# Optimization experiments

Hardware: AMD Instinct MI355X
Metric: run time of the kernel (lower is better)

The kernel has to match this reference:

```python
import jax, jax.numpy as jnp
import numpy as np

DIM = 1024
INNER = DIM // 2
DSTATE = 8
KSZ = 3
DTRANK = max(INNER // 8, 4)
B, L = 4, 4096


def setup_inputs() -> dict:
    key = jax.random.key(0)
    ks = jax.random.split(key, 8)
    s = 0.02
    x = jax.random.normal(ks[0], (B, L, DIM), dtype=jnp.float32)
    W_in = jax.random.normal(ks[1], (DIM, DIM), dtype=jnp.float32) * s
    Kx = jax.random.normal(ks[2], (INNER, 1, KSZ), dtype=jnp.float32) * 0.1
    Kz = jax.random.normal(ks[3], (INNER, 1, KSZ), dtype=jnp.float32) * 0.1
    W_xproj = jax.random.normal(ks[4], (DTRANK + 2 * DSTATE, INNER), dtype=jnp.float32) * s
    W_dt = jax.random.normal(ks[5], (INNER, DTRANK), dtype=jnp.float32) * s
    # dt bias: inverse_softplus of exp(linspace(log dt_min, log dt_max))
    dt_init = jnp.exp(jnp.linspace(jnp.log(0.02), jnp.log(0.2), INNER))
    b_dt = jnp.log(jnp.expm1(dt_init)).astype(jnp.float32)
    A_log = jnp.log(jnp.tile(jnp.arange(1, DSTATE + 1, dtype=jnp.float32), (INNER, 1)))
    D = jnp.ones((INNER,), dtype=jnp.float32)
    W_out = jax.random.normal(ks[6], (DIM, DIM), dtype=jnp.float32) * s
    return {"x": x, "W_in": W_in, "Kx": Kx, "Kz": Kz, "W_xproj": W_xproj,
            "W_dt": W_dt, "b_dt": b_dt, "A_log": A_log, "D": D, "W_out": W_out}


def _dwconv_silu(u, kern):
    # u: [B,L,C], kern: [C,1,K] depthwise (groups=C), 'same' padding
    c = u.shape[-1]
    v = jnp.transpose(u, (0, 2, 1))  # [B,C,L]
    v = jax.lax.conv_general_dilated(v, kern, (1,), [(KSZ // 2, KSZ // 2)],
                                     dimension_numbers=("NCH", "OIH", "NCH"),
                                     feature_group_count=c)
    return jax.nn.silu(jnp.transpose(v, (0, 2, 1)))


def _forward(x, W_in, Kx, Kz, W_xproj, W_dt, b_dt, A_log, D, W_out):
    h = jnp.einsum("bld,ed->ble", x, W_in)  # Linear(dim,dim), no bias
    xb, zb = jnp.split(h, 2, axis=-1)       # [B,L,INNER] each
    xb = _dwconv_silu(xb, Kx)
    zb = _dwconv_silu(zb, Kz)
    proj = jnp.einsum("blc,oc->blo", xb, W_xproj)
    dt_raw = proj[..., :DTRANK]
    b_raw = proj[..., DTRANK:DTRANK + DSTATE]
    c_raw = proj[..., DTRANK + DSTATE:]
    delta = jnp.clip(jax.nn.softplus(jnp.einsum("blr,cr->blc", dt_raw, W_dt) + b_dt), 1e-4, 1.0)  # [B,L,C]
    b_term = jnp.tanh(b_raw)  # [B,L,N]
    c_term = jnp.tanh(c_raw)  # [B,L,N]
    a = jax.nn.softplus(A_log) + 1e-4  # [C,N]
    decay = jnp.clip(jnp.exp(-delta[..., None] * a), 1e-4, 1.0)        # [B,L,C,N]
    drive = (1.0 - decay) * (b_term[:, :, None, :] * xb[..., None])    # [B,L,C,N]

    def step(state, inp):
        dec_t, drv_t, c_t, x_t = inp  # [B,C,N], [B,C,N], [B,N], [B,C]
        state = dec_t * state + drv_t
        y = jnp.sum(state * c_t[:, None, :], axis=-1) + D * x_t  # [B,C]
        return state, y

    tm = lambda t: jnp.moveaxis(t, 1, 0)  # time-major
    state0 = jnp.zeros((x.shape[0], INNER, DSTATE), dtype=jnp.float32)
    _, ys = jax.lax.scan(step, state0, (tm(decay), tm(drive), tm(c_term), tm(xb)))
    y = jnp.moveaxis(ys, 0, 1)  # [B,L,INNER]
    return jnp.einsum("bld,ed->ble", jnp.concatenate([y, zb], axis=-1), W_out)


def reference(x, W_in, Kx, Kz, W_xproj, W_dt, b_dt, A_log, D, W_out):
    return _forward(x, W_in, Kx, Kz, W_xproj, W_dt, b_dt, A_log, D, W_out)
```

## Files before the change

kernel.cpp:

```cpp
#include <hip/hip_runtime.h>


using bf16x8 = __attribute__((ext_vector_type(8))) short;
using f32x4  = __attribute__((ext_vector_type(4))) float;

__device__ __forceinline__ unsigned short f2bf(float f) {
  unsigned int u = __float_as_uint(f);
  u = u + 0x7fffu + ((u >> 16) & 1u);
  return (unsigned short)(u >> 16);
}

__device__ __forceinline__ float fsoftplus(float x) {
  return (x > 15.f) ? x : __logf(1.f + __expf(x));
}

__device__ __forceinline__ float ftanh(float x) {
  float v = fminf(fmaxf(x, -15.f), 15.f);
  float e = __expf(2.f * v);
  return (e - 1.f) / (e + 1.f);
}

__global__ __launch_bounds__(256) void cvt_bf16_kernel(
    const float* __restrict__ in, unsigned short* __restrict__ out, int n4) {
  int i = blockIdx.x * 256 + threadIdx.x;
  if (i < n4) {
    float4 v = ((const float4*)in)[i];
    ushort4 o;
    o.x = f2bf(v.x); o.y = f2bf(v.y); o.z = f2bf(v.z); o.w = f2bf(v.w);
    ((ushort4*)out)[i] = o;
  }
}

__global__ __launch_bounds__(256) void cvt_wxp_kernel(
    const float* __restrict__ Wx, unsigned short* __restrict__ out) {
  int i = blockIdx.x * 256 + threadIdx.x;
  int row = i >> 9;
  out[i] = (row < 80) ? f2bf(Wx[i]) : (unsigned short)0;
}

__global__ __launch_bounds__(256) void gemm_bt_bf16(
    const unsigned short* __restrict__ A,
    const unsigned short* __restrict__ B,
    float* __restrict__ C, int M, int N, int K) {
  __shared__ short As[128 * 32];
  __shared__ short Bs[128 * 32];
  const int m0 = blockIdx.x * 128;
  const int n0 = blockIdx.y * 128;
  const int lane = threadIdx.x & 63;
  const int wv = threadIdx.x >> 6;
  const int wm = (wv >> 1) * 64;
  const int wn = (wv & 1) * 64;
  f32x4 acc[4][4] = {};
  const int row_a = wv * 32 + (lane >> 2);
  const int koff = (lane & 3) * 8;
  const unsigned short* gA = A + (size_t)(m0 + row_a) * K + koff;
  const unsigned short* gB = B + (size_t)(n0 + row_a) * K + koff;
  short* lA = &As[(wv * 32) * 32];
  short* lB = &Bs[(wv * 32) * 32];
  const int r = lane & 15;
  const int q = lane >> 4;
  for (int k0 = 0; k0 < K; k0 += 32) {
    __syncthreads();
    __builtin_amdgcn_global_load_lds((const __attribute__((address_space(1))) void*)(const void*)gA,
                                     (__attribute__((address_space(3))) void*)(void*)lA, 16, 0, 0);
    __builtin_amdgcn_global_load_lds((const __attribute__((address_space(1))) void*)(const void*)(gA + 16 * K),
                                     (__attribute__((address_space(3))) void*)(void*)(lA + 16 * 32), 16, 0, 0);
    __builtin_amdgcn_global_load_lds((const __attribute__((address_space(1))) void*)(const void*)gB,
                                     (__attribute__((address_space(3))) void*)(void*)lB, 16, 0, 0);
    __builtin_amdgcn_global_load_lds((const __attribute__((address_space(1))) void*)(const void*)(gB + 16 * K),
                                     (__attribute__((address_space(3))) void*)(void*)(lB + 16 * 32), 16, 0, 0);
    gA += 32; gB += 32;
    __syncthreads();
    bf16x8 av[4], bv[4];
#pragma unroll
    for (int i = 0; i < 4; ++i)
      av[i] = *(const bf16x8*)&As[(wm + i * 16 + r) * 32 + q * 8];
#pragma unroll
    for (int j = 0; j < 4; ++j)
      bv[j] = *(const bf16x8*)&Bs[(wn + j * 16 + r) * 32 + q * 8];
#pragma unroll
    for (int i = 0; i < 4; ++i)
#pragma unroll
      for (int j = 0; j < 4; ++j)
        acc[i][j] = __builtin_amdgcn_mfma_f32_16x16x32_bf16(av[i], bv[j], acc[i][j], 0, 0, 0);
  }
#pragma unroll
  for (int i = 0; i < 4; ++i)
#pragma unroll
    for (int j = 0; j < 4; ++j)
#pragma unroll
      for (int t = 0; t < 4; ++t)
        C[(size_t)(m0 + wm + i * 16 + q * 4 + t) * N + (n0 + wn + j * 16 + r)] = acc[i][j][t];
}

__device__ __forceinline__ void g256_stage(short* lds, int slot,
    const unsigned short* sp, int ktIdx, int wvLds, int K) {
  const unsigned short* s = sp + ktIdx * 64;
  __builtin_amdgcn_global_load_lds((const __attribute__((address_space(1))) void*)s,
      (__attribute__((address_space(3))) void*)(lds + slot * 8192 + wvLds), 16, 0, 0);
  __builtin_amdgcn_global_load_lds((const __attribute__((address_space(1))) void*)(s + (size_t)64 * K),
      (__attribute__((address_space(3))) void*)(lds + slot * 8192 + 4096 + wvLds), 16, 0, 0);
}

template <int PAR, int MH, int NHLO, bool RA, bool RB, int SSLOT, bool VM, bool HINT>
__device__ __forceinline__ void g256_phase(
    short* lds, int aSlotOff, int bSlotOff, int aoff, int boff, int wvLds,
    bf16x8 (&av)[4][2], bf16x8 (&bv)[4][2], f32x4 (&acc)[8][4],
    const unsigned short* sp, int ktIdx, int K) {
  if (RA) {
#pragma unroll
    for (int ii = 0; ii < 4; ++ii) {
      av[ii][0] = *(const bf16x8*)&lds[PAR * 4 * 8192 + aSlotOff + MH * 4096 + ii * 1024 + aoff];
      av[ii][1] = *(const bf16x8*)&lds[PAR * 4 * 8192 + aSlotOff + MH * 4096 + ii * 1024 + (aoff ^ 32)];
    }
  }
  if (RB) {
#pragma unroll
    for (int jj = 0; jj < 2; ++jj) {
      bv[NHLO + jj][0] = *(const bf16x8*)&lds[(PAR * 4 + 2) * 8192 + bSlotOff + (NHLO + jj) * 1024 + boff];
      bv[NHLO + jj][1] = *(const bf16x8*)&lds[(PAR * 4 + 2) * 8192 + bSlotOff + (NHLO + jj) * 1024 + (boff ^ 32)];
    }
  }
  g256_stage(lds, SSLOT, sp, ktIdx, wvLds, K);
  if (HINT) asm volatile("s_waitcnt lgkmcnt(8)");
  if (VM) asm volatile("s_waitcnt vmcnt(4)" ::: "memory");
  __builtin_amdgcn_s_barrier();
  asm volatile("s_waitcnt lgkmcnt(0)" ::: "memory");
  __builtin_amdgcn_s_setprio(1);
#pragma unroll
  for (int ii = 0; ii < 4; ++ii)
#pragma unroll
    for (int jj = 0; jj < 2; ++jj) {
      acc[MH * 4 + ii][NHLO + jj] = __builtin_amdgcn_mfma_f32_16x16x32_bf16(
          av[ii][0], bv[NHLO + jj][0], acc[MH * 4 + ii][NHLO + jj], 0, 0, 0);
      acc[MH * 4 + ii][NHLO + jj] = __builtin_amdgcn_mfma_f32_16x16x32_bf16(
          av[ii][1], bv[NHLO + jj][1], acc[MH * 4 + ii][NHLO + jj], 0, 0, 0);
    }
  __builtin_amdgcn_s_setprio(0);
  __builtin_amdgcn_s_barrier();
}

__global__ __launch_bounds__(512, 2) void gemm256_bt(
    const unsigned short* __restrict__ A,
    const unsigned short* __restrict__ B,
    float* __restrict__ C, int M, int N, int K) {
  __shared__ short lds[8 * 8192];
  const int nmt = M >> 8;
  const int bid = blockIdx.x;
  const int g = nmt >> 3;
  const int xcd = bid & 7;
  const int loc = bid >> 3;
  const int mtile = xcd * g + (loc % g);
  const int ntile = loc / g;
  const int m0 = mtile << 8, n0 = ntile << 8;
  const int tid = threadIdx.x;
  const int w = tid >> 6, lane = tid & 63;
  const int r = lane & 15, q = lane >> 4;
  const int wrow = w >> 2, wcol = w & 3;
  const int srow = tid >> 3;
  const int scol = ((tid & 7) ^ (srow & 7)) << 3;
  const unsigned short* pA0 = A + (size_t)(m0 + srow) * K + scol;
  const unsigned short* pA1 = A + (size_t)(m0 + 128 + srow) * K + scol;
  const unsigned short* pB0 = B + (size_t)(n0 + srow) * K + scol;
  const unsigned short* pB1 = B + (size_t)(n0 + 128 + srow) * K + scol;
  const int wvLds = w * 512;
  const int aSlotOff = wrow * 8192;
  const int bSlotOff = (wcol >> 1) * 8192;
  const int swzc = (q * 8) ^ ((r & 7) << 3);
  const int aoff = r * 64 + swzc;
  const int boff = (wcol & 1) * 4096 + r * 64 + swzc;
  bf16x8 av[4][2], bv[4][2];
  f32x4 acc[8][4] = {};
  const int NT = K >> 6;
  const int NI = NT >> 1;
  g256_stage(lds, 0, pA0, 0, wvLds, K);
  g256_stage(lds, 1, pA1, 0, wvLds, K);
  g256_stage(lds, 2, pB0, 0, wvLds, K);
  g256_stage(lds, 3, pB1, 0, wvLds, K);
  g256_stage(lds, 6, pB0, 1, wvLds, K);
  g256_stage(lds, 7, pB1, 1, wvLds, K);
  asm volatile("s_waitcnt vmcnt(4)" ::: "memory");
  __builtin_amdgcn_s_barrier();
#pragma unroll 1
  for (int it = 0; it < NI; ++it) {
    const int ktO  = 2 * it + 1;
    const int ktE2 = (2 * it + 2 < NT) ? 2 * it + 2 : NT - 1;
    const int ktO2 = (2 * it + 3 < NT) ? 2 * it + 3 : NT - 1;
    g256_phase<0, 0, 0, true,  true,  4, false, true >(lds, aSlotOff, bSlotOff, aoff, boff, wvLds, av, bv, acc, pA0, ktO,  K);
    g256_phase<0, 0, 2, false, true,  5, false, false>(lds, aSlotOff, bSlotOff, aoff, boff, wvLds, av, bv, acc, pA1, ktO,  K);
    g256_phase<0, 1, 2, true,  false, 2, false, false>(lds, aSlotOff, bSlotOff, aoff, boff, wvLds, av, bv, acc, pB0, ktE2, K);
    g256_phase<0, 1, 0, false, false, 0, true,  false>(lds, aSlotOff, bSlotOff, aoff, boff, wvLds, av, bv, acc, pA0, ktE2, K);
    g256_phase<1, 0, 0, true,  true,  1, false, true >(lds, aSlotOff, bSlotOff, aoff, boff, wvLds, av, bv, acc, pA1, ktE2, K);
    g256_phase<1, 0, 2, false, true,  3, false, false>(lds, aSlotOff, bSlotOff, aoff, boff, wvLds, av, bv, acc, pB1, ktE2, K);
    g256_phase<1, 1, 2, true,  false, 6, false, false>(lds, aSlotOff, bSlotOff, aoff, boff, wvLds, av, bv, acc, pB0, ktO2, K);
    g256_phase<1, 1, 0, false, false, 7, true,  false>(lds, aSlotOff, bSlotOff, aoff, boff, wvLds, av, bv, acc, pB1, ktO2, K);
  }
  asm volatile("s_waitcnt vmcnt(0) lgkmcnt(0)" ::: "memory");
  float* Cw = C + (size_t)(m0 + wrow * 128) * N + n0 + wcol * 64;
#pragma unroll
  for (int ii = 0; ii < 8; ++ii)
#pragma unroll
    for (int jj = 0; jj < 4; ++jj)
#pragma unroll
      for (int t = 0; t < 4; ++t)
        Cw[(size_t)(ii * 16 + q * 4 + t) * N + jj * 16 + r] = acc[ii][jj][t];
}

__global__ __launch_bounds__(256) void conv_silu_kernel(
    const float* __restrict__ h, const float* __restrict__ Kx, const float* __restrict__ Kz,
    float* __restrict__ xb, unsigned short* __restrict__ xbbf,
    unsigned short* __restrict__ cat) {
  int tid = blockIdx.x * 256 + threadIdx.x;
  int ch = tid & 1023;
  int bl = tid >> 10;
  int l = bl & 4095;
  float k0, k1, k2;
  int c;
  if (ch < 512) { c = ch;       k0 = Kx[c * 3]; k1 = Kx[c * 3 + 1]; k2 = Kx[c * 3 + 2]; }
  else          { c = ch - 512; k0 = Kz[c * 3]; k1 = Kz[c * 3 + 1]; k2 = Kz[c * 3 + 2]; }
  size_t idx = (size_t)bl * 1024 + ch;
  float um = (l > 0)    ? h[idx - 1024] : 0.f;
  float u0 = h[idx];
  float up = (l < 4095) ? h[idx + 1024] : 0.f;
  float v = um * k0 + u0 * k1 + up * k2;
  float o = v / (1.f + __expf(-v));
  if (ch < 512) { xb[(size_t)bl * 512 + c] = o; xbbf[(size_t)bl * 512 + c] = f2bf(o); }
  else          cat[idx] = f2bf(o);
}

__global__ __launch_bounds__(256) void prep_dtbc_kernel(
    const float* __restrict__ proj, unsigned short* __restrict__ dtr,
    float* __restrict__ bterm, float* __restrict__ cterm) {
  int i = blockIdx.x * 256 + threadIdx.x;
  int row = i >> 7, col = i & 127;
  float v = proj[i];
  if (col < 64)      dtr[row * 64 + col] = f2bf(v);
  else if (col < 72) bterm[row * 8 + (col - 64)] = ftanh(v);
  else if (col < 80) cterm[row * 8 + (col - 72)] = ftanh(v);
}

__global__ __launch_bounds__(256) void scan_p1(
    const float* __restrict__ draw, const float* __restrict__ bterm,
    const float* __restrict__ xb, const float* __restrict__ A_log,
    const float* __restrict__ bdt,
    float* __restrict__ Aprod, float* __restrict__ Bpart) {
  int tid = threadIdx.x;
  int gid = blockIdx.x;
  int chunk = gid & 127, half = (gid >> 7) & 1, b = gid >> 8;
  int c = half * 256 + tid;
  float4 a0 = *(const float4*)&A_log[c * 8];
  float4 a1 = *(const float4*)&A_log[c * 8 + 4];
  float na[8] = {a0.x, a0.y, a0.z, a0.w, a1.x, a1.y, a1.z, a1.w};
#pragma unroll
  for (int s = 0; s < 8; ++s) na[s] = -(fsoftplus(na[s]) + 1e-4f);
  float bb = bdt[c];
  int l0 = chunk * 32;
  size_t base  = ((size_t)b * 4096 + l0) * 512 + c;
  size_t bbase = ((size_t)b * 4096 + l0) * 8;
  float S[8] = {}, Ap[8] = {1.f, 1.f, 1.f, 1.f, 1.f, 1.f, 1.f, 1.f};
  for (int i = 0; i < 32; ++i) {
    float dr = draw[base] + bb;
    float xv = xb[base];
    float delta = fminf(fmaxf(fsoftplus(dr), 1e-4f), 1.f);
    float4 bt0 = *(const float4*)&bterm[bbase];
    float4 bt1 = *(const float4*)&bterm[bbase + 4];
    float bt[8] = {bt0.x, bt0.y, bt0.z, bt0.w, bt1.x, bt1.y, bt1.z, bt1.w};
#pragma unroll
    for (int s = 0; s < 8; ++s) {
      float dec = fminf(fmaxf(__expf(delta * na[s]), 1e-4f), 1.f);
      float btx = bt[s] * xv;
      S[s] = dec * S[s] + (btx - dec * btx);
      Ap[s] *= dec;
    }
    base += 512; bbase += 8;
  }
  size_t o = (size_t)chunk * 16384 + ((size_t)(b * 512 + c)) * 8;
  *(float4*)&Aprod[o]     = make_float4(Ap[0], Ap[1], Ap[2], Ap[3]);
  *(float4*)&Aprod[o + 4] = make_float4(Ap[4], Ap[5], Ap[6], Ap[7]);
  *(float4*)&Bpart[o]     = make_float4(S[0], S[1], S[2], S[3]);
  *(float4*)&Bpart[o + 4] = make_float4(S[4], S[5], S[6], S[7]);
}

__global__ __launch_bounds__(256) void scan_p2(
    const float* __restrict__ Aprod, const float* __restrict__ Bpart,
    float* __restrict__ initst) {
  int t = blockIdx.x * 256 + threadIdx.x;
  float st = 0.f;
  for (int ch = 0; ch < 128; ++ch) {
    size_t o = (size_t)ch * 16384 + t;
    initst[o] = st;
    st = Aprod[o] * st + Bpart[o];
  }
}

__global__ __launch_bounds__(256) void scan_p3(
    const float* __restrict__ draw, const float* __restrict__ bterm,
    const float* __restrict__ cterm, const float* __restrict__ xb,
    const float* __restrict__ A_log, const float* __restrict__ bdt,
    const float* __restrict__ Dp,
    const float* __restrict__ initst, unsigned short* __restrict__ cat) {
  int tid = threadIdx.x;
  int gid = blockIdx.x;
  int chunk = gid & 127, half = (gid >> 7) & 1, b = gid >> 8;
  int c = half * 256 + tid;
  float4 a0 = *(const float4*)&A_log[c * 8];
  float4 a1 = *(const float4*)&A_log[c * 8 + 4];
  float na[8] = {a0.x, a0.y, a0.z, a0.w, a1.x, a1.y, a1.z, a1.w};
#pragma unroll
  for (int s = 0; s < 8; ++s) na[s] = -(fsoftplus(na[s]) + 1e-4f);
  float bb = bdt[c];
  float Dv = Dp[c];
  size_t o = (size_t)chunk * 16384 + ((size_t)(b * 512 + c)) * 8;
  float4 s0 = *(const float4*)&initst[o];
  float4 s1 = *(const float4*)&initst[o + 4];
  float S[8] = {s0.x, s0.y, s0.z, s0.w, s1.x, s1.y, s1.z, s1.w};
  int l0 = chunk * 32;
  size_t base  = ((size_t)b * 4096 + l0) * 512 + c;
  size_t bbase = ((size_t)b * 4096 + l0) * 8;
  size_t cbase = ((size_t)b * 4096 + l0) * 1024 + c;
  for (int i = 0; i < 32; ++i) {
    float dr = draw[base] + bb;
    float xv = xb[base];
    float delta = fminf(fmaxf(fsoftplus(dr), 1e-4f), 1.f);
    float4 bt0 = *(const float4*)&bterm[bbase];
    float4 bt1 = *(const float4*)&bterm[bbase + 4];
    float4 ct0 = *(const float4*)&cterm[bbase];
    float4 ct1 = *(const float4*)&cterm[bbase + 4];
    float bt[8] = {bt0.x, bt0.y, bt0.z, bt0.w, bt1.x, bt1.y, bt1.z, bt1.w};
    float ct[8] = {ct0.x, ct0.y, ct0.z, ct0.w, ct1.x, ct1.y, ct1.z, ct1.w};
    float acc = Dv * xv;
#pragma unroll
    for (int s = 0; s < 8; ++s) {
      float dec = fminf(fmaxf(__expf(delta * na[s]), 1e-4f), 1.f);
      float btx = bt[s] * xv;
      S[s] = dec * S[s] + (btx - dec * btx);
      acc += S[s] * ct[s];
    }
    cat[cbase] = f2bf(acc);
    base += 512; bbase += 8; cbase += 1024;
  }
}

extern "C" void kernel_launch(void* const* d_in, const int* in_sizes, int n_in,
                              void* d_out, int out_size, void* d_ws, size_t ws_size,
                              hipStream_t stream) {
  (void)in_sizes; (void)n_in; (void)out_size; (void)ws_size;
  const float* x       = (const float*)d_in[0];
  const float* W_in    = (const float*)d_in[1];
  const float* Kx      = (const float*)d_in[2];
  const float* Kz      = (const float*)d_in[3];
  const float* W_xproj = (const float*)d_in[4];
  const float* W_dt    = (const float*)d_in[5];
  const float* b_dt    = (const float*)d_in[6];
  const float* A_log   = (const float*)d_in[7];
  const float* Dp      = (const float*)d_in[8];
  const float* W_out   = (const float*)d_in[9];
  float* out = (float*)d_out;

  char* w = (char*)d_ws;
  unsigned short* xbf  = (unsigned short*)(w);
  float* xb    = (float*)(w + 33554432);
  float* draw  = (float*)(w + 67108864);
  float* bterm = (float*)(w + 100663296);
  float* cterm = (float*)(w + 101187584);
  float* Aprod = (float*)(w + 101711872);
  float* Bpart = (float*)(w + 110100480);
  float* initst = (float*)(w + 118489088);
  unsigned short* winbf  = (unsigned short*)(w + 126877696);
  unsigned short* woutbf = (unsigned short*)(w + 128974848);
  unsigned short* dtr    = (unsigned short*)(w + 131072000);
  unsigned short* wxp_bf = (unsigned short*)(w + 133169152);
  unsigned short* wd_bf  = (unsigned short*)(w + 133300224);
  unsigned short* xbbf = (unsigned short*)Aprod;
  float* proj = draw;
  float* h = out;

  cvt_bf16_kernel<<<16384, 256, 0, stream>>>(x, xbf, 4194304);
  cvt_bf16_kernel<<<1024, 256, 0, stream>>>(W_in, winbf, 262144);
  cvt_bf16_kernel<<<1024, 256, 0, stream>>>(W_out, woutbf, 262144);
  cvt_bf16_kernel<<<32, 256, 0, stream>>>(W_dt, wd_bf, 8192);
  cvt_wxp_kernel<<<256, 256, 0, stream>>>(W_xproj, wxp_bf);

  gemm256_bt<<<256, 512, 0, stream>>>(xbf, winbf, h, 16384, 1024, 1024);

  conv_silu_kernel<<<65536, 256, 0, stream>>>(h, Kx, Kz, xb, xbbf, xbf );

  gemm_bt_bf16<<<dim3(128, 1), 256, 0, stream>>>(xbbf, wxp_bf, proj, 16384, 128, 512);
  prep_dtbc_kernel<<<8192, 256, 0, stream>>>(proj, dtr, bterm, cterm);
  gemm_bt_bf16<<<dim3(128, 4), 256, 0, stream>>>(dtr, wd_bf, draw, 16384, 512, 64);

  scan_p1<<<1024, 256, 0, stream>>>(draw, bterm, xb, A_log, b_dt, Aprod, Bpart);
  scan_p2<<<64, 256, 0, stream>>>(Aprod, Bpart, initst);
  scan_p3<<<1024, 256, 0, stream>>>(draw, bterm, cterm, xb, A_log, b_dt, Dp, initst, xbf );

  gemm256_bt<<<256, 512, 0, stream>>>(xbf, woutbf, out, 16384, 1024, 1024);
}
```

Before: 347.5 us.

## Fuse epilogues into small GEMMs, vectorize conv, and re-pipeline big GEMM LDS reads

The prep_dtbc pass is folded into the x-projection GEMM epilogue, which now writes the bf16 dt rows and the tanh of the B/C terms directly. The softplus and clip for delta move into the dt GEMM epilogue, so the two scan kernels read delta instead of recomputing it. The depthwise conv+SiLU kernel now handles four channels per thread with float4 loads, and scan_p2 batches its loads eight chunks at a time. The 256-tile GEMM is re-pipelined so LDS fragment reads for the next phase are issued after the current MFMAs and one more stage is prefetched. Together these aim to cut kernel launches, intermediate traffic and repeated transcendental math, but the GEMM reordering raises register pressure and depends on correct waitcnt bookkeeping.

```diff
diff --git a/kernel.cpp b/kernel.cpp
--- a/kernel.cpp
+++ b/kernel.cpp
@@ -38,9 +38,73 @@
   out[i] = (row < 80) ? f2bf(Wx[i]) : (unsigned short)0;
 }
 
-__global__ __launch_bounds__(256) void gemm_bt_bf16(
+
+__global__ __launch_bounds__(256) void gemm_proj128(
     const unsigned short* __restrict__ A,
     const unsigned short* __restrict__ B,
+    unsigned short* __restrict__ dtr, float* __restrict__ bterm,
+    float* __restrict__ cterm, int M, int N, int K) {
+  __shared__ short As[128 * 32];
+  __shared__ short Bs[128 * 32];
+  const int m0 = blockIdx.x * 128;
+  const int lane = threadIdx.x & 63;
+  const int wv = threadIdx.x >> 6;
+  const int wm = (wv >> 1) * 64;
+  const int wn = (wv & 1) * 64;
+  f32x4 acc[4][4] = {};
+  const int row_a = wv * 32 + (lane >> 2);
+  const int koff = (lane & 3) * 8;
+  const unsigned short* gA = A + (size_t)(m0 + row_a) * K + koff;
+  const unsigned short* gB = B + (size_t)row_a * K + koff;
+  short* lA = &As[(wv * 32) * 32];
+  short* lB = &Bs[(wv * 32) * 32];
+  const int r = lane & 15;
+  const int q = lane >> 4;
+  for (int k0 = 0; k0 < K; k0 += 32) {
+    __syncthreads();
+    __builtin_amdgcn_global_load_lds((const __attribute__((address_space(1))) void*)(const void*)gA,
+                                     (__attribute__((address_space(3))) void*)(void*)lA, 16, 0, 0);
+    __builtin_amdgcn_global_load_lds((const __attribute__((address_space(1))) void*)(const void*)(gA + 16 * K),
+                                     (__attribute__((address_space(3))) void*)(void*)(lA + 16 * 32), 16, 0, 0);
+    __builtin_amdgcn_global_load_lds((const __attribute__((address_space(1))) void*)(const void*)gB,
+                                     (__attribute__((address_space(3))) void*)(void*)lB, 16, 0, 0);
+    __builtin_amdgcn_global_load_lds((const __attribute__((address_space(1))) void*)(const void*)(gB + 16 * K),
+                                     (__attribute__((address_space(3))) void*)(void*)(lB + 16 * 32), 16, 0, 0);
+    gA += 32; gB += 32;
+    __syncthreads();
+    bf16x8 av[4], bv[4];
+#pragma unroll
+    for (int i = 0; i < 4; ++i)
+      av[i] = *(const bf16x8*)&As[(wm + i * 16 + r) * 32 + q * 8];
+#pragma unroll
+    for (int j = 0; j < 4; ++j)
+      bv[j] = *(const bf16x8*)&Bs[(wn + j * 16 + r) * 32 + q * 8];
+#pragma unroll
+    for (int i = 0; i < 4; ++i)
+#pragma unroll
+      for (int j = 0; j < 4; ++j)
+        acc[i][j] = __builtin_amdgcn_mfma_f32_16x16x32_bf16(av[i], bv[j], acc[i][j], 0, 0, 0);
+  }
+#pragma unroll
+  for (int i = 0; i < 4; ++i)
+#pragma unroll
+    for (int j = 0; j < 4; ++j) {
+      const int col = wn + j * 16 + r;
+#pragma unroll
+      for (int t = 0; t < 4; ++t) {
+        const int row = m0 + wm + i * 16 + q * 4 + t;
+        float v = acc[i][j][t];
+        if (col < 64)      dtr[(size_t)row * 64 + col] = f2bf(v);
+        else if (col < 72) bterm[(size_t)row * 8 + (col - 64)] = ftanh(v);
+        else if (col < 80) cterm[(size_t)row * 8 + (col - 72)] = ftanh(v);
+      }
+    }
+}
+
+__global__ __launch_bounds__(256) void gemm_dt128(
+    const unsigned short* __restrict__ A,
+    const unsigned short* __restrict__ B,
+    const float* __restrict__ bdt,
     float* __restrict__ C, int M, int N, int K) {
   __shared__ short As[128 * 32];
   __shared__ short Bs[128 * 32];
@@ -85,12 +149,18 @@
         acc[i][j] = __builtin_amdgcn_mfma_f32_16x16x32_bf16(av[i], bv[j], acc[i][j], 0, 0, 0);
   }
 #pragma unroll
-  for (int i = 0; i < 4; ++i)
-#pragma unroll
-    for (int j = 0; j < 4; ++j)
-#pragma unroll
-      for (int t = 0; t < 4; ++t)
-        C[(size_t)(m0 + wm + i * 16 + q * 4 + t) * N + (n0 + wn + j * 16 + r)] = acc[i][j][t];
+  for (int j = 0; j < 4; ++j) {
+    const int col = n0 + wn + j * 16 + r;
+    const float bb = bdt[col];
+#pragma unroll
+    for (int i = 0; i < 4; ++i)
+#pragma unroll
+      for (int t = 0; t < 4; ++t) {
+        float v = acc[i][j][t] + bb;
+        float delta = fminf(fmaxf(fsoftplus(v), 1e-4f), 1.f);
+        C[(size_t)(m0 + wm + i * 16 + q * 4 + t) * N + col] = delta;
+      }
+  }
 }
 
 __device__ __forceinline__ void g256_stage(short* lds, int slot,
@@ -102,41 +172,51 @@
       (__attribute__((address_space(3))) void*)(lds + slot * 8192 + 4096 + wvLds), 16, 0, 0);
 }
 
-template <int PAR, int MH, int NHLO, bool RA, bool RB, int SSLOT, bool VM, bool HINT>
+template <int MP, int MH, int NL, int SSLOT, bool VM, int RK, int RP>
 __device__ __forceinline__ void g256_phase(
     short* lds, int aSlotOff, int bSlotOff, int aoff, int boff, int wvLds,
     bf16x8 (&av)[4][2], bf16x8 (&bv)[4][2], f32x4 (&acc)[8][4],
     const unsigned short* sp, int ktIdx, int K) {
-  if (RA) {
+  g256_stage(lds, SSLOT, sp, ktIdx, wvLds, K);
+  if (VM) asm volatile("s_waitcnt vmcnt(6)" ::: "memory");
+  __builtin_amdgcn_s_barrier();
+  __builtin_amdgcn_s_setprio(1);
+#pragma unroll
+  for (int ii = 0; ii < 4; ++ii)
+#pragma unroll
+    for (int jj = 0; jj < 2; ++jj) {
+      acc[MH * 4 + ii][NL + jj] = __builtin_amdgcn_mfma_f32_16x16x32_bf16(
+          av[ii][0], bv[NL + jj][0], acc[MH * 4 + ii][NL + jj], 0, 0, 0);
+      acc[MH * 4 + ii][NL + jj] = __builtin_amdgcn_mfma_f32_16x16x32_bf16(
+          av[ii][1], bv[NL + jj][1], acc[MH * 4 + ii][NL + jj], 0, 0, 0);
+    }
+  __builtin_amdgcn_s_setprio(0);
+  if (RK == 2) {
 #pragma unroll
     for (int ii = 0; ii < 4; ++ii) {
-      av[ii][0] = *(const bf16x8*)&lds[PAR * 4 * 8192 + aSlotOff + MH * 4096 + ii * 1024 + aoff];
-      av[ii][1] = *(const bf16x8*)&lds[PAR * 4 * 8192 + aSlotOff + MH * 4096 + ii * 1024 + (aoff ^ 32)];
-    }
-  }
-  if (RB) {
+      av[ii][0] = *(const bf16x8*)&lds[RP * 4 * 8192 + aSlotOff + 4096 + ii * 1024 + aoff];
+      av[ii][1] = *(const bf16x8*)&lds[RP * 4 * 8192 + aSlotOff + 4096 + ii * 1024 + (aoff ^ 32)];
+    }
+  }
+  if (RK >= 3) {
+#pragma unroll
+    for (int ii = 0; ii < 4; ++ii) {
+      av[ii][0] = *(const bf16x8*)&lds[RP * 4 * 8192 + aSlotOff + ii * 1024 + aoff];
+      av[ii][1] = *(const bf16x8*)&lds[RP * 4 * 8192 + aSlotOff + ii * 1024 + (aoff ^ 32)];
+    }
 #pragma unroll
     for (int jj = 0; jj < 2; ++jj) {
-      bv[NHLO + jj][0] = *(const bf16x8*)&lds[(PAR * 4 + 2) * 8192 + bSlotOff + (NHLO + jj) * 1024 + boff];
-      bv[NHLO + jj][1] = *(const bf16x8*)&lds[(PAR * 4 + 2) * 8192 + bSlotOff + (NHLO + jj) * 1024 + (boff ^ 32)];
-    }
-  }
-  g256_stage(lds, SSLOT, sp, ktIdx, wvLds, K);
-  if (HINT) asm volatile("s_waitcnt lgkmcnt(8)");
-  if (VM) asm volatile("s_waitcnt vmcnt(4)" ::: "memory");
-  __builtin_amdgcn_s_barrier();
-  asm volatile("s_waitcnt lgkmcnt(0)" ::: "memory");
-  __builtin_amdgcn_s_setprio(1);
-#pragma unroll
-  for (int ii = 0; ii < 4; ++ii)
-#pragma unroll
-    for (int jj = 0; jj < 2; ++jj) {
-      acc[MH * 4 + ii][NHLO + jj] = __builtin_amdgcn_mfma_f32_16x16x32_bf16(
-          av[ii][0], bv[NHLO + jj][0], acc[MH * 4 + ii][NHLO + jj], 0, 0, 0);
-      acc[MH * 4 + ii][NHLO + jj] = __builtin_amdgcn_mfma_f32_16x16x32_bf16(
-          av[ii][1], bv[NHLO + jj][1], acc[MH * 4 + ii][NHLO + jj], 0, 0, 0);
-    }
-  __builtin_amdgcn_s_setprio(0);
+      bv[jj][0] = *(const bf16x8*)&lds[(RP * 4 + 2) * 8192 + bSlotOff + jj * 1024 + boff];
+      bv[jj][1] = *(const bf16x8*)&lds[(RP * 4 + 2) * 8192 + bSlotOff + jj * 1024 + (boff ^ 32)];
+    }
+  }
+  if (RK == 1 || RK == 4) {
+#pragma unroll
+    for (int jj = 2; jj < 4; ++jj) {
+      bv[jj][0] = *(const bf16x8*)&lds[(RP * 4 + 2) * 8192 + bSlotOff + jj * 1024 + boff];
+      bv[jj][1] = *(const bf16x8*)&lds[(RP * 4 + 2) * 8192 + bSlotOff + jj * 1024 + (boff ^ 32)];
+    }
+  }
   __builtin_amdgcn_s_barrier();
 }
 
@@ -177,23 +257,34 @@
   g256_stage(lds, 1, pA1, 0, wvLds, K);
   g256_stage(lds, 2, pB0, 0, wvLds, K);
   g256_stage(lds, 3, pB1, 0, wvLds, K);
+  g256_stage(lds, 4, pA0, 1, wvLds, K);
   g256_stage(lds, 6, pB0, 1, wvLds, K);
   g256_stage(lds, 7, pB1, 1, wvLds, K);
-  asm volatile("s_waitcnt vmcnt(4)" ::: "memory");
+  asm volatile("s_waitcnt vmcnt(6)" ::: "memory");
   __builtin_amdgcn_s_barrier();
+#pragma unroll
+  for (int ii = 0; ii < 4; ++ii) {
+    av[ii][0] = *(const bf16x8*)&lds[aSlotOff + ii * 1024 + aoff];
+    av[ii][1] = *(const bf16x8*)&lds[aSlotOff + ii * 1024 + (aoff ^ 32)];
+  }
+#pragma unroll
+  for (int jj = 0; jj < 2; ++jj) {
+    bv[jj][0] = *(const bf16x8*)&lds[2 * 8192 + bSlotOff + jj * 1024 + boff];
+    bv[jj][1] = *(const bf16x8*)&lds[2 * 8192 + bSlotOff + jj * 1024 + (boff ^ 32)];
+  }
 #pragma unroll 1
   for (int it = 0; it < NI; ++it) {
-    const int ktO  = 2 * it + 1;
-    const int ktE2 = (2 * it + 2 < NT) ? 2 * it + 2 : NT - 1;
-    const int ktO2 = (2 * it + 3 < NT) ? 2 * it + 3 : NT - 1;
-    g256_phase<0, 0, 0, true,  true,  4, false, true >(lds, aSlotOff, bSlotOff, aoff, boff, wvLds, av, bv, acc, pA0, ktO,  K);
-    g256_phase<0, 0, 2, false, true,  5, false, false>(lds, aSlotOff, bSlotOff, aoff, boff, wvLds, av, bv, acc, pA1, ktO,  K);
-    g256_phase<0, 1, 2, true,  false, 2, false, false>(lds, aSlotOff, bSlotOff, aoff, boff, wvLds, av, bv, acc, pB0, ktE2, K);
-    g256_phase<0, 1, 0, false, false, 0, true,  false>(lds, aSlotOff, bSlotOff, aoff, boff, wvLds, av, bv, acc, pA0, ktE2, K);
-    g256_phase<1, 0, 0, true,  true,  1, false, true >(lds, aSlotOff, bSlotOff, aoff, boff, wvLds, av, bv, acc, pA1, ktE2, K);
-    g256_phase<1, 0, 2, false, true,  3, false, false>(lds, aSlotOff, bSlotOff, aoff, boff, wvLds, av, bv, acc, pB1, ktE2, K);
-    g256_phase<1, 1, 2, true,  false, 6, false, false>(lds, aSlotOff, bSlotOff, aoff, boff, wvLds, av, bv, acc, pB0, ktO2, K);
-    g256_phase<1, 1, 0, false, false, 7, true,  false>(lds, aSlotOff, bSlotOff, aoff, boff, wvLds, av, bv, acc, pB1, ktO2, K);
+    const int ktO = 2 * it + 1;
+    const int kt2 = (2 * it + 2 < NT) ? 2 * it + 2 : NT - 1;
+    const int kt3 = (2 * it + 3 < NT) ? 2 * it + 3 : NT - 1;
+    g256_phase<0,0,0, 5, false, 1, 0>(lds, aSlotOff, bSlotOff, aoff, boff, wvLds, av, bv, acc, pA1, ktO, K);
+    g256_phase<0,0,2, 2, false, 2, 0>(lds, aSlotOff, bSlotOff, aoff, boff, wvLds, av, bv, acc, pB0, kt2, K);
+    g256_phase<0,1,2, 3, false, 0, 0>(lds, aSlotOff, bSlotOff, aoff, boff, wvLds, av, bv, acc, pB1, kt2, K);
+    g256_phase<0,1,0, 0, true,  4, 1>(lds, aSlotOff, bSlotOff, aoff, boff, wvLds, av, bv, acc, pA0, kt2, K);
+    g256_phase<1,0,0, 1, false, 0, 0>(lds, aSlotOff, bSlotOff, aoff, boff, wvLds, av, bv, acc, pA1, kt2, K);
+    g256_phase<1,0,2, 6, false, 2, 1>(lds, aSlotOff, bSlotOff, aoff, boff, wvLds, av, bv, acc, pB0, kt3, K);
+    g256_phase<1,1,2, 7, false, 0, 0>(lds, aSlotOff, bSlotOff, aoff, boff, wvLds, av, bv, acc, pB1, kt3, K);
+    g256_phase<1,1,0, 4, true,  3, 0>(lds, aSlotOff, bSlotOff, aoff, boff, wvLds, av, bv, acc, pA0, kt3, K);
   }
   asm volatile("s_waitcnt vmcnt(0) lgkmcnt(0)" ::: "memory");
   float* Cw = C + (size_t)(m0 + wrow * 128) * N + n0 + wcol * 64;
@@ -206,43 +297,45 @@
         Cw[(size_t)(ii * 16 + q * 4 + t) * N + jj * 16 + r] = acc[ii][jj][t];
 }
 
-__global__ __launch_bounds__(256) void conv_silu_kernel(
+__global__ __launch_bounds__(256) void conv_silu_v4(
     const float* __restrict__ h, const float* __restrict__ Kx, const float* __restrict__ Kz,
     float* __restrict__ xb, unsigned short* __restrict__ xbbf,
     unsigned short* __restrict__ cat) {
   int tid = blockIdx.x * 256 + threadIdx.x;
-  int ch = tid & 1023;
-  int bl = tid >> 10;
+  int c4 = (tid & 255) << 2;
+  int bl = tid >> 8;
   int l = bl & 4095;
-  float k0, k1, k2;
-  int c;
-  if (ch < 512) { c = ch;       k0 = Kx[c * 3]; k1 = Kx[c * 3 + 1]; k2 = Kx[c * 3 + 2]; }
-  else          { c = ch - 512; k0 = Kz[c * 3]; k1 = Kz[c * 3 + 1]; k2 = Kz[c * 3 + 2]; }
-  size_t idx = (size_t)bl * 1024 + ch;
-  float um = (l > 0)    ? h[idx - 1024] : 0.f;
-  float u0 = h[idx];
-  float up = (l < 4095) ? h[idx + 1024] : 0.f;
-  float v = um * k0 + u0 * k1 + up * k2;
-  float o = v / (1.f + __expf(-v));
-  if (ch < 512) { xb[(size_t)bl * 512 + c] = o; xbbf[(size_t)bl * 512 + c] = f2bf(o); }
-  else          cat[idx] = f2bf(o);
-}
-
-__global__ __launch_bounds__(256) void prep_dtbc_kernel(
-    const float* __restrict__ proj, unsigned short* __restrict__ dtr,
-    float* __restrict__ bterm, float* __restrict__ cterm) {
-  int i = blockIdx.x * 256 + threadIdx.x;
-  int row = i >> 7, col = i & 127;
-  float v = proj[i];
-  if (col < 64)      dtr[row * 64 + col] = f2bf(v);
-  else if (col < 72) bterm[row * 8 + (col - 64)] = ftanh(v);
-  else if (col < 80) cterm[row * 8 + (col - 72)] = ftanh(v);
+  const float* Kp; int c;
+  if (c4 < 512) { Kp = Kx; c = c4; } else { Kp = Kz; c = c4 - 512; }
+  const float4* K4 = (const float4*)(Kp + c * 3);
+  float4 ka = K4[0], kb = K4[1], kc = K4[2];
+  size_t idx = (size_t)bl * 1024 + c4;
+  float4 zero = make_float4(0.f, 0.f, 0.f, 0.f);
+  float4 um = (l > 0)    ? *(const float4*)(h + idx - 1024) : zero;
+  float4 u0 = *(const float4*)(h + idx);
+  float4 up = (l < 4095) ? *(const float4*)(h + idx + 1024) : zero;
+  float v0 = um.x * ka.x + u0.x * ka.y + up.x * ka.z;
+  float v1 = um.y * ka.w + u0.y * kb.x + up.y * kb.y;
+  float v2 = um.z * kb.z + u0.z * kb.w + up.z * kc.x;
+  float v3 = um.w * kc.y + u0.w * kc.z + up.w * kc.w;
+  float o0 = v0 / (1.f + __expf(-v0));
+  float o1 = v1 / (1.f + __expf(-v1));
+  float o2 = v2 / (1.f + __expf(-v2));
+  float o3 = v3 / (1.f + __expf(-v3));
+  ushort4 ob;
+  ob.x = f2bf(o0); ob.y = f2bf(o1); ob.z = f2bf(o2); ob.w = f2bf(o3);
+  if (c4 < 512) {
+    size_t xo = (size_t)bl * 512 + c4;
+    *(float4*)(xb + xo) = make_float4(o0, o1, o2, o3);
+    *(ushort4*)(xbbf + xo) = ob;
+  } else {
+    *(ushort4*)(cat + idx) = ob;
+  }
 }
 
 __global__ __launch_bounds__(256) void scan_p1(
-    const float* __restrict__ draw, const float* __restrict__ bterm,
+    const float* __restrict__ delta_in, const float* __restrict__ bterm,
     const float* __restrict__ xb, const float* __restrict__ A_log,
-    const float* __restrict__ bdt,
     float* __restrict__ Aprod, float* __restrict__ Bpart) {
   int tid = threadIdx.x;
   int gid = blockIdx.x;
@@ -253,15 +346,13 @@
   float na[8] = {a0.x, a0.y, a0.z, a0.w, a1.x, a1.y, a1.z, a1.w};
 #pragma unroll
   for (int s = 0; s < 8; ++s) na[s] = -(fsoftplus(na[s]) + 1e-4f);
-  float bb = bdt[c];
   int l0 = chunk * 32;
   size_t base  = ((size_t)b * 4096 + l0) * 512 + c;
   size_t bbase = ((size_t)b * 4096 + l0) * 8;
   float S[8] = {}, Ap[8] = {1.f, 1.f, 1.f, 1.f, 1.f, 1.f, 1.f, 1.f};
   for (int i = 0; i < 32; ++i) {
-    float dr = draw[base] + bb;
+    float delta = delta_in[base];
     float xv = xb[base];
-    float delta = fminf(fmaxf(fsoftplus(dr), 1e-4f), 1.f);
     float4 bt0 = *(const float4*)&bterm[bbase];
     float4 bt1 = *(const float4*)&bterm[bbase + 4];
     float bt[8] = {bt0.x, bt0.y, bt0.z, bt0.w, bt1.x, bt1.y, bt1.z, bt1.w};
@@ -286,18 +377,26 @@
     float* __restrict__ initst) {
   int t = blockIdx.x * 256 + threadIdx.x;
   float st = 0.f;
-  for (int ch = 0; ch < 128; ++ch) {
-    size_t o = (size_t)ch * 16384 + t;
-    initst[o] = st;
-    st = Aprod[o] * st + Bpart[o];
+  for (int cb = 0; cb < 128; cb += 8) {
+    float a[8], bb[8];
+#pragma unroll
+    for (int j = 0; j < 8; ++j) {
+      size_t o = (size_t)(cb + j) * 16384 + t;
+      a[j] = Aprod[o]; bb[j] = Bpart[o];
+    }
+#pragma unroll
+    for (int j = 0; j < 8; ++j) {
+      size_t o = (size_t)(cb + j) * 16384 + t;
+      initst[o] = st;
+      st = a[j] * st + bb[j];
+    }
   }
 }
 
 __global__ __launch_bounds__(256) void scan_p3(
-    const float* __restrict__ draw, const float* __restrict__ bterm,
+    const float* __restrict__ delta_in, const float* __restrict__ bterm,
     const float* __restrict__ cterm, const float* __restrict__ xb,
-    const float* __restrict__ A_log, const float* __restrict__ bdt,
-    const float* __restrict__ Dp,
+    const float* __restrict__ A_log, const float* __restrict__ Dp,
     const float* __restrict__ initst, unsigned short* __restrict__ cat) {
   int tid = threadIdx.x;
   int gid = blockIdx.x;
@@ -308,7 +407,6 @@
   float na[8] = {a0.x, a0.y, a0.z, a0.w, a1.x, a1.y, a1.z, a1.w};
 #pragma unroll
   for (int s = 0; s < 8; ++s) na[s] = -(fsoftplus(na[s]) + 1e-4f);
-  float bb = bdt[c];
   float Dv = Dp[c];
   size_t o = (size_t)chunk * 16384 + ((size_t)(b * 512 + c)) * 8;
   float4 s0 = *(const float4*)&initst[o];
@@ -319,9 +417,8 @@
   size_t bbase = ((size_t)b * 4096 + l0) * 8;
   size_t cbase = ((size_t)b * 4096 + l0) * 1024 + c;
   for (int i = 0; i < 32; ++i) {
-    float dr = draw[base] + bb;
+    float delta = delta_in[base];
     float xv = xb[base];
-    float delta = fminf(fmaxf(fsoftplus(dr), 1e-4f), 1.f);
     float4 bt0 = *(const float4*)&bterm[bbase];
     float4 bt1 = *(const float4*)&bterm[bbase + 4];
     float4 ct0 = *(const float4*)&cterm[bbase];
@@ -372,7 +469,6 @@
   unsigned short* wxp_bf = (unsigned short*)(w + 133169152);
   unsigned short* wd_bf  = (unsigned short*)(w + 133300224);
   unsigned short* xbbf = (unsigned short*)Aprod;
-  float* proj = draw;
   float* h = out;
 
   cvt_bf16_kernel<<<16384, 256, 0, stream>>>(x, xbf, 4194304);
@@ -383,15 +479,14 @@
 
   gemm256_bt<<<256, 512, 0, stream>>>(xbf, winbf, h, 16384, 1024, 1024);
 
-  conv_silu_kernel<<<65536, 256, 0, stream>>>(h, Kx, Kz, xb, xbbf, xbf );
-
-  gemm_bt_bf16<<<dim3(128, 1), 256, 0, stream>>>(xbbf, wxp_bf, proj, 16384, 128, 512);
-  prep_dtbc_kernel<<<8192, 256, 0, stream>>>(proj, dtr, bterm, cterm);
-  gemm_bt_bf16<<<dim3(128, 4), 256, 0, stream>>>(dtr, wd_bf, draw, 16384, 512, 64);
-
-  scan_p1<<<1024, 256, 0, stream>>>(draw, bterm, xb, A_log, b_dt, Aprod, Bpart);
+  conv_silu_v4<<<16384, 256, 0, stream>>>(h, Kx, Kz, xb, xbbf, xbf );
+
+  gemm_proj128<<<128, 256, 0, stream>>>(xbbf, wxp_bf, dtr, bterm, cterm, 16384, 128, 512);
+  gemm_dt128<<<dim3(128, 4), 256, 0, stream>>>(dtr, wd_bf, b_dt, draw, 16384, 512, 64);
+
+  scan_p1<<<1024, 256, 0, stream>>>(draw, bterm, xb, A_log, Aprod, Bpart);
   scan_p2<<<64, 256, 0, stream>>>(Aprod, Bpart, initst);
-  scan_p3<<<1024, 256, 0, stream>>>(draw, bterm, cterm, xb, A_log, b_dt, Dp, initst, xbf );
+  scan_p3<<<1024, 256, 0, stream>>>(draw, bterm, cterm, xb, A_log, Dp, initst, xbf );
 
   gemm256_bt<<<256, 512, 0, stream>>>(xbf, woutbf, out, 16384, 1024, 1024);
 }
```

After: 338.9 us. 2.5% less time.
